# Kernel optimization log

Measured on AMD Instinct MI355X. Metric: run time of the kernel, lower is better.

The kernel has to match this reference:

```python
import jax, jax.numpy as jnp
import numpy as np

B, K, C, H, W = 16, 32, 256, 80, 80
NH, HD = 8, 32          # num_heads, head_dim (C = NH*HD)
S = 4                   # fixed roi_align sampling grid per 1x1 output bin
EPS = 1e-5


def _bn(x, g, b, m, v):
    # inference-mode BatchNorm2d, NCHW
    s = g / jnp.sqrt(v + EPS)
    return x * s[None, :, None, None] + (b - m * s)[None, :, None, None]


def _bilinear(feat, ys, xs):
    # feat [B,C,H,W]; ys,xs [B,K,S,S] -> [B,K,S,S,C], torchvision roi_align semantics
    Hh, Ww = feat.shape[2], feat.shape[3]
    valid = (ys >= -1.0) & (ys <= Hh) & (xs >= -1.0) & (xs <= Ww)
    y = jnp.clip(ys, 0.0, Hh - 1.0)
    x = jnp.clip(xs, 0.0, Ww - 1.0)
    y0 = jnp.floor(y); x0 = jnp.floor(x)
    y0i = y0.astype(jnp.int32); x0i = x0.astype(jnp.int32)
    y1i = jnp.minimum(y0i + 1, Hh - 1); x1i = jnp.minimum(x0i + 1, Ww - 1)
    ly = y - y0; lx = x - x0; hy = 1.0 - ly; hx = 1.0 - lx
    bidx = jnp.arange(feat.shape[0])[:, None, None, None]
    g = lambda yi, xi: feat[bidx, :, yi, xi]  # -> [B,K,S,S,C]
    val = ((hy * hx)[..., None] * g(y0i, x0i) + (hy * lx)[..., None] * g(y0i, x1i)
           + (ly * hx)[..., None] * g(y1i, x0i) + (ly * lx)[..., None] * g(y1i, x1i))
    return val * valid[..., None].astype(val.dtype)


def _roi_align_1x1(feat, boxes):
    # boxes [B,K,4] normalized xyxy; spatial_scale = 1.0 in the source
    Hh, Ww = feat.shape[2], feat.shape[3]
    sc = jnp.asarray([Ww - 1, Hh - 1, Ww - 1, Hh - 1], feat.dtype)
    ab = boxes * sc
    x1, y1, x2, y2 = ab[..., 0], ab[..., 1], ab[..., 2], ab[..., 3]
    rw = jnp.maximum(x2 - x1, 1.0)
    rh = jnp.maximum(y2 - y1, 1.0)
    grid = (jnp.arange(S, dtype=feat.dtype) + 0.5) / S
    ys = y1[..., None] + grid * rh[..., None]   # [B,K,S]
    xs = x1[..., None] + grid * rw[..., None]
    ys2, xs2 = jnp.broadcast_arrays(ys[..., :, None], xs[..., None, :])  # [B,K,S,S]
    vals = _bilinear(feat, ys2, xs2)            # [B,K,S,S,C]
    return vals.mean(axis=(2, 3)).reshape(feat.shape[0] * boxes.shape[1], -1)


def _gat(nodes, wq, bq, wk, bkp, wv, bv, scale, wo, bo, ln_g, ln_b):
    Bk = nodes.shape[0]
    q = (nodes @ wq.T + bq).reshape(Bk, NH, HD)
    k = (nodes @ wk.T + bkp).reshape(Bk, NH, HD)
    v = (nodes @ wv.T + bv).reshape(Bk, NH, HD)
    scores = jnp.einsum('ihd,jhd->ijh', q, k) * scale
    attn = jax.nn.softmax(scores, axis=1)       # softmax over keys j
    msg = jnp.einsum('ijh,jhd->ihd', attn, v).reshape(Bk, NH * HD)
    y = nodes + msg @ wo.T + bo
    mu = y.mean(-1, keepdims=True)
    var = ((y - mu) ** 2).mean(-1, keepdims=True)
    return (y - mu) / jnp.sqrt(var + EPS) * ln_g + ln_b


def _forward(x, boxes, conv_w, conv_b, bn1_g, bn1_b, bn1_m, bn1_v,
             wq, bq, wk, bkp, wv, bv, scale, wo, bo, ln_g, ln_b,
             rec_w, rec_b, bn2_g, bn2_b, bn2_m, bn2_v):
    feat = jax.lax.conv_general_dilated(
        x, conv_w, (1, 1), 'SAME',
        dimension_numbers=('NCHW', 'OIHW', 'NCHW')) + conv_b[None, :, None, None]
    feat = _bn(feat, bn1_g, bn1_b, bn1_m, bn1_v)
    feat = feat * jax.nn.sigmoid(feat)          # SiLU
    nodes = _roi_align_1x1(feat, boxes)         # [B*K, C]
    enh = _gat(nodes, wq, bq, wk, bkp, wv, bv, scale, wo, bo, ln_g, ln_b)
    f = enh.reshape(B, K, C)
    wts = jax.nn.softmax(f.mean(-1), axis=1)    # [B,K]
    weighted = jnp.einsum('bkc,bk->bc', f, wts)
    # out map is spatially constant -> 1x1 conv + BN collapse to per-sample affine
    y = weighted @ rec_w[:, :, 0, 0].T + rec_b
    s = bn2_g / jnp.sqrt(bn2_v + EPS)
    y = y * s + (bn2_b - bn2_m * s)
    return x + y[:, :, None, None]


def setup_inputs() -> dict:
    key = jax.random.key(0)
    ks = jax.random.split(key, 10)
    x = jax.random.normal(ks[0], (B, C, H, W), jnp.float32)
    bx = jax.random.uniform(ks[1], (B, K, 4), jnp.float32)
    bx = bx.at[:, :, 2:].add(bx[:, :, :2])      # xy2 += xy1
    boxes = jnp.clip(bx, 0.0, 1.0)
    w = lambda k, shp: jax.random.normal(k, shp, jnp.float32) * 0.02
    return {
        'x': x, 'boxes': boxes,
        'conv_w': w(ks[2], (C, C, 3, 3)), 'conv_b': jnp.zeros((C,), jnp.float32),
        'bn1_g': jnp.ones((C,), jnp.float32), 'bn1_b': jnp.zeros((C,), jnp.float32),
        'bn1_m': jnp.zeros((C,), jnp.float32), 'bn1_v': jnp.ones((C,), jnp.float32),
        'wq': w(ks[3], (C, C)), 'bq': jnp.zeros((C,), jnp.float32),
        'wk': w(ks[4], (C, C)), 'bkp': jnp.zeros((C,), jnp.float32),
        'wv': w(ks[5], (C, C)), 'bv': jnp.zeros((C,), jnp.float32),
        'scale': jnp.asarray(1.0 / np.sqrt(HD), jnp.float32),
        'wo': w(ks[6], (C, C)), 'bo': jnp.zeros((C,), jnp.float32),
        'ln_g': jnp.ones((C,), jnp.float32), 'ln_b': jnp.zeros((C,), jnp.float32),
        'rec_w': w(ks[7], (C, C, 1, 1)), 'rec_b': jnp.zeros((C,), jnp.float32),
        'bn2_g': jnp.ones((C,), jnp.float32), 'bn2_b': jnp.zeros((C,), jnp.float32),
        'bn2_m': jnp.zeros((C,), jnp.float32), 'bn2_v': jnp.ones((C,), jnp.float32),
    }


def reference(x, boxes, conv_w, conv_b, bn1_g, bn1_b, bn1_m, bn1_v,
              wq, bq, wk, bkp, wv, bv, scale, wo, bo, ln_g, ln_b,
              rec_w, rec_b, bn2_g, bn2_b, bn2_m, bn2_v):
    return _forward(x, boxes, conv_w, conv_b, bn1_g, bn1_b, bn1_m, bn1_v,
                    wq, bq, wk, bkp, wv, bv, scale, wo, bo, ln_g, ln_b,
                    rec_w, rec_b, bn2_g, bn2_b, bn2_m, bn2_v)
```

## Files before the change

### kernel.cpp

```cpp
#include <hip/hip_runtime.h>

#define EPSV 1e-5f

typedef __attribute__((ext_vector_type(8))) short short8v;
typedef __attribute__((ext_vector_type(4))) float f32x4;

static __device__ __forceinline__ unsigned short f2bf(float f) {
  unsigned int u = __float_as_uint(f);
  u += 0x7fff + ((u >> 16) & 1);
  return (unsigned short)(u >> 16);
}
static __device__ __forceinline__ float bf2f(unsigned short h) {
  return __uint_as_float(((unsigned int)h) << 16);
}

static __device__ __forceinline__ void glds16(const void* g, void* l) {
  __builtin_amdgcn_global_load_lds(
      (const __attribute__((address_space(1))) void*)g,
      (__attribute__((address_space(3))) void*)l, 16, 0, 0);
}

__global__ __launch_bounds__(256) void prep_convw_kernel(
    const float* __restrict__ cw, unsigned short* __restrict__ Wr,
    float* __restrict__ zpad)
{
  if (blockIdx.x == 0) zpad[threadIdx.x] = 0.f;
  int idx = blockIdx.x * 256 + threadIdx.x;
  if (idx >= 9 * 8 * 256 * 32) return;
  int cil = idx & 31;
  int rest = idx >> 5;
  int co = rest & 255;
  int tcc = rest >> 8;
  int cc = tcc & 7;
  int t = tcc >> 3;
  int dy = t / 3, dx = t - dy * 3;
  int ci = cc * 32 + cil;
  Wr[idx] = f2bf(cw[((co * 256 + ci) * 3 + dy) * 3 + dx]);
}

__global__ __launch_bounds__(256) void prep_transpose_kernel(
    const float* __restrict__ wq, const float* __restrict__ wk,
    const float* __restrict__ wv, const float* __restrict__ wo,
    const float* __restrict__ rec, float* __restrict__ wT)
{
  int idx = blockIdx.x * 256 + threadIdx.x;
  if (idx >= 5 * 65536) return;
  int m = idx >> 16;
  int e = idx & 65535;
  int ci = e >> 8, co = e & 255;
  const float* src = (m == 0) ? wq : (m == 1) ? wk : (m == 2) ? wv : (m == 3) ? wo : rec;
  wT[idx] = src[co * 256 + ci];
}

__global__ __launch_bounds__(256) void prep_nhwc_kernel(
    const float* __restrict__ x, unsigned short* __restrict__ xin)
{
  int blk = blockIdx.x;
  int b = blk / 80, y = blk - b * 80;
  __shared__ unsigned short t[80 * 257];
  const float* src = x + (size_t)b * 256 * 6400 + y * 80;
  for (int e = threadIdx.x; e < 256 * 20; e += 256) {
    int c = e / 20;
    int px4 = e - c * 20;
    f32x4 v = *(const f32x4*)&src[(size_t)c * 6400 + px4 * 4];
#pragma unroll
    for (int j = 0; j < 4; ++j)
      t[(px4 * 4 + j) * 257 + c] = f2bf(v[j]);
  }
  __syncthreads();
  unsigned short* dst = xin + (size_t)blk * 80 * 256;
  for (int e = threadIdx.x; e < 80 * 32; e += 256) {
    int px = e >> 5;
    int c8 = e & 31;
    short8v v;
#pragma unroll
    for (int j = 0; j < 8; ++j) v[j] = t[px * 257 + c8 * 8 + j];
    *(short8v*)&dst[px * 256 + c8 * 8] = v;
  }
}

__global__ __launch_bounds__(256, 2) void roiconv_kernel(
    const unsigned short* __restrict__ xin,
    const float* __restrict__ boxes,
    const float* __restrict__ convb,
    const float* __restrict__ bn1g, const float* __restrict__ bn1b,
    const float* __restrict__ bn1m, const float* __restrict__ bn1v,
    const unsigned short* __restrict__ Wr,
    float* __restrict__ nodes)
{
  const int bid = blockIdx.x;
  const int n = (bid & 7) * 64 + (bid >> 3);
  const int b = n >> 5;
  const int tid = threadIdx.x;
  const int w = tid >> 6, lane = tid & 63;
  const int bq = lane >> 4, r16 = lane & 15;

  __shared__ __align__(16) char lds[65792];
  float* wcoef = (float*)(lds + 65536);
  const int IN0 = 0, IN1 = 4096, W0 = 8192, W1 = 24576;

  const int px = tid >> 2;
  const float* bx = boxes + n * 4;
  float x1 = bx[0] * 79.f, y1 = bx[1] * 79.f, x2 = bx[2] * 79.f, y2 = bx[3] * 79.f;
  float rwd = fmaxf(x2 - x1, 1.f), rh = fmaxf(y2 - y1, 1.f);
  int s = px >> 2;
  int sy = s >> 2, sx = s & 3;
  float yy = y1 + (sy + 0.5f) * 0.25f * rh;
  float xx = x1 + (sx + 0.5f) * 0.25f * rwd;
  bool valid = (yy >= -1.f) && (yy <= 80.f) && (xx >= -1.f) && (xx <= 80.f);
  float yc = fminf(fmaxf(yy, 0.f), 79.f), xc = fminf(fmaxf(xx, 0.f), 79.f);
  float y0f = floorf(yc), x0f = floorf(xc);
  int y0i = (int)y0f, x0i = (int)x0f;
  int y1i = min(y0i + 1, 79), x1i = min(x0i + 1, 79);
  float ly = yc - y0f, lx = xc - x0f, hy = 1.f - ly, hx = 1.f - lx;
  int py = (px & 2) ? y1i : y0i;
  int pxx = (px & 1) ? x1i : x0i;
  if ((tid & 3) == 0)
    wcoef[px] = ((px & 2) ? ly : hy) * ((px & 1) ? lx : hx) *
                (valid ? 0.0625f : 0.f);

  const int chunk = (tid & 3) ^ ((px >> 1) & 3);
  unsigned ioff[9];
#pragma unroll
  for (int t = 0; t < 9; ++t) {
    int dy = t / 3, dx = t - dy * 3;
    int cy = py + dy - 1, cx = pxx + dx - 1;
    bool ok = ((unsigned)cy < 80u) && ((unsigned)cx < 80u);
    ioff[t] = ok ? (unsigned)((((b * 80 + cy) * 80 + cx) * 256 + chunk * 8) * 2)
                 : 52428800u;
  }
  unsigned woff[4];
#pragma unroll
  for (int i = 0; i < 4; ++i) {
    int s2 = tid + (i << 8);
    int wco = s2 >> 2;
    int wch = (s2 & 3) ^ ((wco >> 1) & 3);
    woff[i] = (unsigned)((wco * 32 + wch * 8) * 2);
  }
  const int laneoff = r16 * 64 + ((bq ^ ((r16 >> 1) & 3)) << 4);
  const char* xinb = (const char*)xin;
  const char* Wrb = (const char*)Wr;

  f32x4 acc[4][4];
#pragma unroll
  for (int i = 0; i < 4; ++i)
#pragma unroll
    for (int j = 0; j < 4; ++j)
      acc[i][j] = (f32x4){0.f, 0.f, 0.f, 0.f};

  glds16(xinb + ioff[0], lds + IN0 + ((w << 6) << 4));
#pragma unroll
  for (int i = 0; i < 4; ++i)
    glds16(Wrb + woff[i], lds + W0 + (((i << 8) + (w << 6)) << 4));
  __syncthreads();

  for (int cc = 0; cc < 8; ++cc) {
#pragma unroll
    for (int t = 0; t < 9; ++t) {
      const int step = cc * 9 + t;
      const char* inb = lds + ((step & 1) ? IN1 : IN0);
      const char* wb  = lds + ((step & 1) ? W1 : W0);
      char* innx = lds + ((step & 1) ? IN0 : IN1);
      char* wbn  = lds + ((step & 1) ? W0 : W1);
      if (step < 71) {
        const int nt = (t == 8) ? 0 : t + 1;
        const int ncc = (t == 8) ? cc + 1 : cc;
        glds16(xinb + ioff[nt] + ncc * 64, innx + ((w << 6) << 4));
        const char* wg = Wrb + ((size_t)(nt * 8 + ncc) << 14);
#pragma unroll
        for (int i = 0; i < 4; ++i)
          glds16(wg + woff[i], wbn + (((i << 8) + (w << 6)) << 4));
      }
      const char* pa = inb + laneoff;
      const char* pw = wb + w * 4096 + laneoff;
      short8v af0 = *(const short8v*)(pa);
      short8v af1 = *(const short8v*)(pa + 1024);
      short8v af2 = *(const short8v*)(pa + 2048);
      short8v af3 = *(const short8v*)(pa + 3072);
      short8v wf0 = *(const short8v*)(pw);
      short8v wf1 = *(const short8v*)(pw + 1024);
      short8v wf2 = *(const short8v*)(pw + 2048);
      short8v wf3 = *(const short8v*)(pw + 3072);
      __builtin_amdgcn_s_setprio(1);
      acc[0][0] = __builtin_amdgcn_mfma_f32_16x16x32_bf16(af0, wf0, acc[0][0], 0, 0, 0);
      acc[0][1] = __builtin_amdgcn_mfma_f32_16x16x32_bf16(af0, wf1, acc[0][1], 0, 0, 0);
      acc[0][2] = __builtin_amdgcn_mfma_f32_16x16x32_bf16(af0, wf2, acc[0][2], 0, 0, 0);
      acc[0][3] = __builtin_amdgcn_mfma_f32_16x16x32_bf16(af0, wf3, acc[0][3], 0, 0, 0);
      acc[1][0] = __builtin_amdgcn_mfma_f32_16x16x32_bf16(af1, wf0, acc[1][0], 0, 0, 0);
      acc[1][1] = __builtin_amdgcn_mfma_f32_16x16x32_bf16(af1, wf1, acc[1][1], 0, 0, 0);
      acc[1][2] = __builtin_amdgcn_mfma_f32_16x16x32_bf16(af1, wf2, acc[1][2], 0, 0, 0);
      acc[1][3] = __builtin_amdgcn_mfma_f32_16x16x32_bf16(af1, wf3, acc[1][3], 0, 0, 0);
      acc[2][0] = __builtin_amdgcn_mfma_f32_16x16x32_bf16(af2, wf0, acc[2][0], 0, 0, 0);
      acc[2][1] = __builtin_amdgcn_mfma_f32_16x16x32_bf16(af2, wf1, acc[2][1], 0, 0, 0);
      acc[2][2] = __builtin_amdgcn_mfma_f32_16x16x32_bf16(af2, wf2, acc[2][2], 0, 0, 0);
      acc[2][3] = __builtin_amdgcn_mfma_f32_16x16x32_bf16(af2, wf3, acc[2][3], 0, 0, 0);
      acc[3][0] = __builtin_amdgcn_mfma_f32_16x16x32_bf16(af3, wf0, acc[3][0], 0, 0, 0);
      acc[3][1] = __builtin_amdgcn_mfma_f32_16x16x32_bf16(af3, wf1, acc[3][1], 0, 0, 0);
      acc[3][2] = __builtin_amdgcn_mfma_f32_16x16x32_bf16(af3, wf2, acc[3][2], 0, 0, 0);
      acc[3][3] = __builtin_amdgcn_mfma_f32_16x16x32_bf16(af3, wf3, acc[3][3], 0, 0, 0);
      __builtin_amdgcn_s_setprio(0);
      __syncthreads();
    }
  }

  float* epf = (float*)lds;
#pragma unroll
  for (int cf = 0; cf < 4; ++cf) {
    int co = w * 64 + cf * 16 + r16;
    float sc = bn1g[co] / sqrtf(bn1v[co] + EPSV);
    float sh = bn1b[co] - bn1m[co] * sc;
    float cb = convb[co];
#pragma unroll
    for (int mf = 0; mf < 4; ++mf) {
#pragma unroll
      for (int rg = 0; rg < 4; ++rg) {
        int pxo = mf * 16 + bq * 4 + rg;
        float v = (acc[mf][cf][rg] + cb) * sc + sh;
        v = v / (1.f + __expf(-v));
        epf[pxo * 256 + co] = v;
      }
    }
  }
  __syncthreads();
  const int c = tid;
  float val = 0.f;
#pragma unroll
  for (int p = 0; p < 64; ++p)
    val += wcoef[p] * epf[p * 256 + c];
  nodes[n * 256 + c] = val;
}

__global__ __launch_bounds__(256) void qkv_kernel(
    const float* __restrict__ nodes, const float* __restrict__ wT,
    const float* __restrict__ bq, const float* __restrict__ bk,
    const float* __restrict__ bv,
    float* __restrict__ q, float* __restrict__ k, float* __restrict__ v)
{
  const int blk = blockIdx.x;
  const int co = threadIdx.x;
  __shared__ float nd[8][256];
  for (int i = threadIdx.x; i < 2048; i += 256)
    nd[i >> 8][i & 255] = nodes[blk * 2048 + i];
  __syncthreads();
  float aq[8] = {0,0,0,0,0,0,0,0};
  float ak[8] = {0,0,0,0,0,0,0,0};
  float av[8] = {0,0,0,0,0,0,0,0};
  const float* wqT = wT;
  const float* wkT = wT + 65536;
  const float* wvT = wT + 131072;
  for (int ci = 0; ci < 256; ++ci) {
    float wq_ = wqT[ci * 256 + co];
    float wk_ = wkT[ci * 256 + co];
    float wv_ = wvT[ci * 256 + co];
#pragma unroll
    for (int r = 0; r < 8; ++r) {
      float nv = nd[r][ci];
      aq[r] += nv * wq_;
      ak[r] += nv * wk_;
      av[r] += nv * wv_;
    }
  }
  float bq_ = bq[co], bk_ = bk[co], bv_ = bv[co];
#pragma unroll
  for (int r = 0; r < 8; ++r) {
    int n = blk * 8 + r;
    q[n * 256 + co] = aq[r] + bq_;
    k[n * 256 + co] = ak[r] + bk_;
    v[n * 256 + co] = av[r] + bv_;
  }
}

__global__ __launch_bounds__(256) void attn_kernel(
    const float* __restrict__ q, const float* __restrict__ k,
    const float* __restrict__ v, const float* __restrict__ nodes,
    const float* __restrict__ woT, const float* __restrict__ bo,
    const float* __restrict__ lng, const float* __restrict__ lnb,
    const float* __restrict__ scale_p, float* __restrict__ enh)
{
  const int i = blockIdx.x;
  const int tid = threadIdx.x;
  const float scale = scale_p[0];
  __shared__ __align__(16) float qs[256];
  __shared__ float sc[512 * 8];
  __shared__ float msgs[256];
  __shared__ float r1[4], r2[4];
  qs[tid] = q[i * 256 + tid];
  __syncthreads();
  {
    const int h = tid & 7, jl = tid >> 3;
    for (int jc = 0; jc < 16; ++jc) {
      int j = jc * 32 + jl;
      const f32x4* kr = (const f32x4*)(k + (size_t)j * 256 + h * 32);
      const f32x4* qr = (const f32x4*)(qs + h * 32);
      float s = 0.f;
#pragma unroll
      for (int d4 = 0; d4 < 8; ++d4) {
        f32x4 kv = kr[d4], qv = qr[d4];
        s += kv.x * qv.x + kv.y * qv.y + kv.z * qv.z + kv.w * qv.w;
      }
      sc[j * 8 + h] = s * scale;
    }
  }
  __syncthreads();
  const int hh = tid >> 5, l32 = tid & 31;
  float mx = -1e30f;
  for (int j = l32; j < 512; j += 32) mx = fmaxf(mx, sc[j * 8 + hh]);
#pragma unroll
  for (int o = 1; o < 32; o <<= 1) mx = fmaxf(mx, __shfl_xor(mx, o, 32));
  float sum = 0.f;
  for (int j = l32; j < 512; j += 32) {
    float e = __expf(sc[j * 8 + hh] - mx);
    sc[j * 8 + hh] = e;
    sum += e;
  }
#pragma unroll
  for (int o = 1; o < 32; o <<= 1) sum += __shfl_xor(sum, o, 32);
  float inv = 1.f / sum;
  __syncthreads();
  {
    const int d = l32;
    float m = 0.f;
    for (int j = 0; j < 512; ++j)
      m += sc[j * 8 + hh] * v[(size_t)j * 256 + hh * 32 + d];
    msgs[hh * 32 + d] = m * inv;
  }
  __syncthreads();
  const int co = tid;
  float yv = nodes[i * 256 + co] + bo[co];
  for (int ci = 0; ci < 256; ++ci)
    yv += msgs[ci] * woT[ci * 256 + co];
  float s1 = yv, s2 = yv * yv;
#pragma unroll
  for (int o = 1; o < 64; o <<= 1) { s1 += __shfl_xor(s1, o); s2 += __shfl_xor(s2, o); }
  if ((tid & 63) == 0) { r1[tid >> 6] = s1; r2[tid >> 6] = s2; }
  __syncthreads();
  float S1 = r1[0] + r1[1] + r1[2] + r1[3];
  float S2 = r2[0] + r2[1] + r2[2] + r2[3];
  float mu = S1 * (1.f / 256.f);
  float var = S2 * (1.f / 256.f) - mu * mu;
  float nrm = (yv - mu) * rsqrtf(var + EPSV);
  enh[i * 256 + co] = nrm * lng[co] + lnb[co];
}

__global__ __launch_bounds__(256) void final_kernel(
    const float* __restrict__ enh, const float* __restrict__ recT,
    const float* __restrict__ recb,
    const float* __restrict__ bn2g, const float* __restrict__ bn2b,
    const float* __restrict__ bn2m, const float* __restrict__ bn2v,
    float* __restrict__ yfin)
{
  const int b = blockIdx.x;
  const int tid = threadIdx.x;
  const int wv = tid >> 6, l = tid & 63;
  __shared__ float rm[32], wts[32], wgt[256];
  for (int kk = wv; kk < 32; kk += 4) {
    const float* er = enh + (size_t)(b * 32 + kk) * 256;
    float s = er[l] + er[l + 64] + er[l + 128] + er[l + 192];
#pragma unroll
    for (int o = 1; o < 64; o <<= 1) s += __shfl_xor(s, o);
    if (l == 0) rm[kk] = s * (1.f / 256.f);
  }
  __syncthreads();
  if (tid < 32) {
    float m = rm[tid];
    float mx = m;
#pragma unroll
    for (int o = 1; o < 32; o <<= 1) mx = fmaxf(mx, __shfl_xor(mx, o, 32));
    float e = __expf(m - mx);
    float sm = e;
#pragma unroll
    for (int o = 1; o < 32; o <<= 1) sm += __shfl_xor(sm, o, 32);
    wts[tid] = e / sm;
  }
  __syncthreads();
  float wsum = 0.f;
  for (int kk = 0; kk < 32; ++kk)
    wsum += enh[(size_t)(b * 32 + kk) * 256 + tid] * wts[kk];
  wgt[tid] = wsum;
  __syncthreads();
  const int co = tid;
  float yv = recb[co];
  for (int ci = 0; ci < 256; ++ci)
    yv += wgt[ci] * recT[ci * 256 + co];
  float s = bn2g[co] / sqrtf(bn2v[co] + EPSV);
  yfin[b * 256 + co] = yv * s + (bn2b[co] - bn2m[co] * s);
}

__global__ __launch_bounds__(256) void add_kernel(
    const float* __restrict__ x, const float* __restrict__ yfin,
    float* __restrict__ out)
{
  const int bc = blockIdx.x;
  const float a = yfin[bc];
  const f32x4* xp = (const f32x4*)(x + (size_t)bc * 6400);
  f32x4* op = (f32x4*)(out + (size_t)bc * 6400);
  for (int i = threadIdx.x; i < 1600; i += 256) {
    f32x4 v = xp[i];
    v.x += a; v.y += a; v.z += a; v.w += a;
    op[i] = v;
  }
}

extern "C" void kernel_launch(void* const* d_in, const int* in_sizes, int n_in,
                              void* d_out, int out_size, void* d_ws, size_t ws_size,
                              hipStream_t stream)
{
  const float* x      = (const float*)d_in[0];
  const float* boxes  = (const float*)d_in[1];
  const float* conv_w = (const float*)d_in[2];
  const float* conv_b = (const float*)d_in[3];
  const float* bn1g   = (const float*)d_in[4];
  const float* bn1b   = (const float*)d_in[5];
  const float* bn1m   = (const float*)d_in[6];
  const float* bn1v   = (const float*)d_in[7];
  const float* wq     = (const float*)d_in[8];
  const float* bq     = (const float*)d_in[9];
  const float* wk     = (const float*)d_in[10];
  const float* bkp    = (const float*)d_in[11];
  const float* wv     = (const float*)d_in[12];
  const float* bv     = (const float*)d_in[13];
  const float* scale  = (const float*)d_in[14];
  const float* wo     = (const float*)d_in[15];
  const float* bo     = (const float*)d_in[16];
  const float* lng    = (const float*)d_in[17];
  const float* lnb    = (const float*)d_in[18];
  const float* rec_w  = (const float*)d_in[19];
  const float* rec_b  = (const float*)d_in[20];
  const float* bn2g   = (const float*)d_in[21];
  const float* bn2b   = (const float*)d_in[22];
  const float* bn2m   = (const float*)d_in[23];
  const float* bn2v   = (const float*)d_in[24];
  float* out = (float*)d_out;

  char* ws = (char*)d_ws;
  unsigned short* Wr   = (unsigned short*)(ws);
  float* wT    = (float*)(ws + 53608448);
  float* nodes = (float*)(ws + 54919168);
  float* qb    = nodes + 131072;
  float* kb    = qb + 131072;
  float* vb    = kb + 131072;
  float* enh   = vb + 131072;
  float* yfin  = enh + 131072;

  unsigned short* xin = (unsigned short*)d_out;
  float* zpad = (float*)((char*)d_out + 52428800);

  hipLaunchKernelGGL(prep_convw_kernel, dim3(2304), dim3(256), 0, stream,
                     conv_w, Wr, zpad);
  hipLaunchKernelGGL(prep_transpose_kernel, dim3(1280), dim3(256), 0, stream,
                     wq, wk, wv, wo, rec_w, wT);
  hipLaunchKernelGGL(prep_nhwc_kernel, dim3(1280), dim3(256), 0, stream, x, xin);
  hipLaunchKernelGGL(roiconv_kernel, dim3(512), dim3(256), 0, stream,
                     xin, boxes, conv_b, bn1g, bn1b, bn1m, bn1v, Wr, nodes);
  hipLaunchKernelGGL(qkv_kernel, dim3(64), dim3(256), 0, stream,
                     nodes, wT, bq, bkp, bv, qb, kb, vb);
  hipLaunchKernelGGL(attn_kernel, dim3(512), dim3(256), 0, stream,
                     qb, kb, vb, nodes, wT + 3 * 65536, bo, lng, lnb, scale, enh);
  hipLaunchKernelGGL(final_kernel, dim3(16), dim3(256), 0, stream,
                     enh, wT + 4 * 65536, rec_b, bn2g, bn2b, bn2m, bn2v, yfin);
  hipLaunchKernelGGL(add_kernel, dim3(4096), dim3(256), 0, stream, x, yfin, out);
}
```

Before: 208.0 us.

## Fuse prep kernels, shrink roiconv LDS, split attention into per-head and out-proj kernels

Merges the three preprocessing kernels into one launch that dispatches on block index. The roiconv epilogue buffer is stored as bf16 with a padded stride, which cuts shared memory so three blocks can fit per CU. The per-query attention kernel is replaced by a per-head kernel that stages K/V for 16 queries in swizzled LDS. A separate kernel then handles the output projection and LayerNorm over 8 rows per block. The trade-offs are an extra launch, a msgs buffer round trip through memory, and bf16 rounding of the softmax probabilities and epilogue activations.

```diff
diff --git a/kernel.cpp b/kernel.cpp
--- a/kernel.cpp
+++ b/kernel.cpp
@@ -20,66 +20,61 @@
       (__attribute__((address_space(3))) void*)l, 16, 0, 0);
 }
 
-__global__ __launch_bounds__(256) void prep_convw_kernel(
+__global__ __launch_bounds__(256) void prep_fused_kernel(
+    const float* __restrict__ x, unsigned short* __restrict__ xin,
     const float* __restrict__ cw, unsigned short* __restrict__ Wr,
-    float* __restrict__ zpad)
-{
-  if (blockIdx.x == 0) zpad[threadIdx.x] = 0.f;
-  int idx = blockIdx.x * 256 + threadIdx.x;
-  if (idx >= 9 * 8 * 256 * 32) return;
-  int cil = idx & 31;
-  int rest = idx >> 5;
-  int co = rest & 255;
-  int tcc = rest >> 8;
-  int cc = tcc & 7;
-  int t = tcc >> 3;
-  int dy = t / 3, dx = t - dy * 3;
-  int ci = cc * 32 + cil;
-  Wr[idx] = f2bf(cw[((co * 256 + ci) * 3 + dy) * 3 + dx]);
-}
-
-__global__ __launch_bounds__(256) void prep_transpose_kernel(
+    float* __restrict__ zpad,
     const float* __restrict__ wq, const float* __restrict__ wk,
     const float* __restrict__ wv, const float* __restrict__ wo,
     const float* __restrict__ rec, float* __restrict__ wT)
 {
-  int idx = blockIdx.x * 256 + threadIdx.x;
-  if (idx >= 5 * 65536) return;
-  int m = idx >> 16;
-  int e = idx & 65535;
-  int ci = e >> 8, co = e & 255;
-  const float* src = (m == 0) ? wq : (m == 1) ? wk : (m == 2) ? wv : (m == 3) ? wo : rec;
-  wT[idx] = src[co * 256 + ci];
-}
-
-__global__ __launch_bounds__(256) void prep_nhwc_kernel(
-    const float* __restrict__ x, unsigned short* __restrict__ xin)
-{
-  int blk = blockIdx.x;
-  int b = blk / 80, y = blk - b * 80;
   __shared__ unsigned short t[80 * 257];
-  const float* src = x + (size_t)b * 256 * 6400 + y * 80;
-  for (int e = threadIdx.x; e < 256 * 20; e += 256) {
-    int c = e / 20;
-    int px4 = e - c * 20;
-    f32x4 v = *(const f32x4*)&src[(size_t)c * 6400 + px4 * 4];
-#pragma unroll
-    for (int j = 0; j < 4; ++j)
-      t[(px4 * 4 + j) * 257 + c] = f2bf(v[j]);
-  }
-  __syncthreads();
-  unsigned short* dst = xin + (size_t)blk * 80 * 256;
-  for (int e = threadIdx.x; e < 80 * 32; e += 256) {
-    int px = e >> 5;
-    int c8 = e & 31;
-    short8v v;
-#pragma unroll
-    for (int j = 0; j < 8; ++j) v[j] = t[px * 257 + c8 * 8 + j];
-    *(short8v*)&dst[px * 256 + c8 * 8] = v;
-  }
-}
-
-__global__ __launch_bounds__(256, 2) void roiconv_kernel(
+  const int bid = blockIdx.x;
+  if (bid < 1280) {
+    int b = bid / 80, y = bid - b * 80;
+    const float* src = x + (size_t)b * 256 * 6400 + y * 80;
+    for (int e = threadIdx.x; e < 256 * 20; e += 256) {
+      int c = e / 20;
+      int px4 = e - c * 20;
+      f32x4 v = *(const f32x4*)&src[(size_t)c * 6400 + px4 * 4];
+#pragma unroll
+      for (int j = 0; j < 4; ++j)
+        t[(px4 * 4 + j) * 257 + c] = f2bf(v[j]);
+    }
+    __syncthreads();
+    unsigned short* dst = xin + (size_t)bid * 80 * 256;
+    for (int e = threadIdx.x; e < 80 * 32; e += 256) {
+      int px = e >> 5;
+      int c8 = e & 31;
+      short8v v;
+#pragma unroll
+      for (int j = 0; j < 8; ++j) v[j] = t[px * 257 + c8 * 8 + j];
+      *(short8v*)&dst[px * 256 + c8 * 8] = v;
+    }
+  } else if (bid < 3584) {
+    if (bid == 1280) zpad[threadIdx.x] = 0.f;
+    int idx = (bid - 1280) * 256 + threadIdx.x;
+    int cil = idx & 31;
+    int rest = idx >> 5;
+    int co = rest & 255;
+    int tcc = rest >> 8;
+    int cc = tcc & 7;
+    int tt = tcc >> 3;
+    int dy = tt / 3, dx = tt - dy * 3;
+    int ci = cc * 32 + cil;
+    Wr[idx] = f2bf(cw[((co * 256 + ci) * 3 + dy) * 3 + dx]);
+  } else {
+    int idx = (bid - 3584) * 256 + threadIdx.x;
+    int m = idx >> 16;
+    int e = idx & 65535;
+    int ci = e >> 8, co = e & 255;
+    const float* src = (m == 0) ? wq : (m == 1) ? wk : (m == 2) ? wv
+                     : (m == 3) ? wo : rec;
+    wT[idx] = src[co * 256 + ci];
+  }
+}
+
+__global__ __launch_bounds__(256, 3) void roiconv_kernel(
     const unsigned short* __restrict__ xin,
     const float* __restrict__ boxes,
     const float* __restrict__ convb,
@@ -95,8 +90,8 @@
   const int w = tid >> 6, lane = tid & 63;
   const int bq = lane >> 4, r16 = lane & 15;
 
-  __shared__ __align__(16) char lds[65792];
-  float* wcoef = (float*)(lds + 65536);
+  __shared__ __align__(16) char lds[41216];
+  float* wcoef = (float*)(lds + 40960);
   const int IN0 = 0, IN1 = 4096, W0 = 8192, W1 = 24576;
 
   const int px = tid >> 2;
@@ -203,7 +198,7 @@
     }
   }
 
-  float* epf = (float*)lds;
+  unsigned short* ep = (unsigned short*)lds;
 #pragma unroll
   for (int cf = 0; cf < 4; ++cf) {
     int co = w * 64 + cf * 16 + r16;
@@ -217,7 +212,7 @@
         int pxo = mf * 16 + bq * 4 + rg;
         float v = (acc[mf][cf][rg] + cb) * sc + sh;
         v = v / (1.f + __expf(-v));
-        epf[pxo * 256 + co] = v;
+        ep[pxo * 264 + co] = f2bf(v);
       }
     }
   }
@@ -226,7 +221,7 @@
   float val = 0.f;
 #pragma unroll
   for (int p = 0; p < 64; ++p)
-    val += wcoef[p] * epf[p * 256 + c];
+    val += wcoef[p] * bf2f(ep[p * 264 + c]);
   nodes[n * 256 + c] = val;
 }
 
@@ -270,76 +265,128 @@
   }
 }
 
-__global__ __launch_bounds__(256) void attn_kernel(
+__global__ __launch_bounds__(256) void attn_mh_kernel(
     const float* __restrict__ q, const float* __restrict__ k,
-    const float* __restrict__ v, const float* __restrict__ nodes,
+    const float* __restrict__ v, const float* __restrict__ scale_p,
+    float* __restrict__ msgs)
+{
+  const int bid = blockIdx.x;
+  const int h = bid & 7, qc = bid >> 3;
+  const int q0 = qc * 16;
+  const int tid = threadIdx.x;
+  __shared__ __align__(16) float Kh[512 * 32];
+  __shared__ __align__(16) float Vh[512 * 32];
+  __shared__ unsigned short pb[16 * 512];
+
+  for (int idx = tid; idx < 4096; idx += 256) {
+    int j = idx >> 3, part = idx & 7;
+    int chs = part ^ (j & 7);
+    *(f32x4*)&Kh[j * 32 + chs * 4] =
+        *(const f32x4*)&k[(size_t)j * 256 + h * 32 + part * 4];
+    *(f32x4*)&Vh[j * 32 + chs * 4] =
+        *(const f32x4*)&v[(size_t)j * 256 + h * 32 + part * 4];
+  }
+  const int qi = tid >> 4, l = tid & 15;
+  f32x4 qr[8];
+#pragma unroll
+  for (int p = 0; p < 8; ++p)
+    qr[p] = *(const f32x4*)&q[(size_t)(q0 + qi) * 256 + h * 32 + p * 4];
+  const float scale = scale_p[0];
+  __syncthreads();
+
+  float pj[32];
+  float mx = -1e30f;
+#pragma unroll
+  for (int jj = 0; jj < 32; ++jj) {
+    int j = jj * 16 + l;
+    const float* kr = &Kh[j * 32];
+    int sw = j & 7;
+    float s = 0.f;
+#pragma unroll
+    for (int p = 0; p < 8; ++p) {
+      f32x4 kv = *(const f32x4*)&kr[(p ^ sw) * 4];
+      s += kv.x * qr[p].x + kv.y * qr[p].y + kv.z * qr[p].z + kv.w * qr[p].w;
+    }
+    s *= scale;
+    pj[jj] = s;
+    mx = fmaxf(mx, s);
+  }
+#pragma unroll
+  for (int o = 1; o < 16; o <<= 1) mx = fmaxf(mx, __shfl_xor(mx, o, 16));
+  float sum = 0.f;
+#pragma unroll
+  for (int jj = 0; jj < 32; ++jj) {
+    float e = __expf(pj[jj] - mx);
+    pj[jj] = e;
+    sum += e;
+  }
+#pragma unroll
+  for (int o = 1; o < 16; o <<= 1) sum += __shfl_xor(sum, o, 16);
+  float inv = 1.f / sum;
+#pragma unroll
+  for (int jj = 0; jj < 32; ++jj)
+    pb[qi * 512 + jj * 16 + l] = f2bf(pj[jj] * inv);
+  __syncthreads();
+
+  float m0 = 0.f, m1 = 0.f;
+  const unsigned short* pq = &pb[qi * 512];
+  for (int j = 0; j < 512; ++j) {
+    float p = bf2f(pq[j]);
+    int chs = (l >> 1) ^ (j & 7);
+    const float* vr = &Vh[j * 32 + chs * 4 + ((2 * l) & 3)];
+    m0 += p * vr[0];
+    m1 += p * vr[1];
+  }
+  float* mo = &msgs[(size_t)(q0 + qi) * 256 + h * 32 + 2 * l];
+  mo[0] = m0;
+  mo[1] = m1;
+}
+
+__global__ __launch_bounds__(256) void outln_kernel(
+    const float* __restrict__ msgs, const float* __restrict__ nodes,
     const float* __restrict__ woT, const float* __restrict__ bo,
     const float* __restrict__ lng, const float* __restrict__ lnb,
-    const float* __restrict__ scale_p, float* __restrict__ enh)
-{
-  const int i = blockIdx.x;
-  const int tid = threadIdx.x;
-  const float scale = scale_p[0];
-  __shared__ __align__(16) float qs[256];
-  __shared__ float sc[512 * 8];
-  __shared__ float msgs[256];
-  __shared__ float r1[4], r2[4];
-  qs[tid] = q[i * 256 + tid];
-  __syncthreads();
-  {
-    const int h = tid & 7, jl = tid >> 3;
-    for (int jc = 0; jc < 16; ++jc) {
-      int j = jc * 32 + jl;
-      const f32x4* kr = (const f32x4*)(k + (size_t)j * 256 + h * 32);
-      const f32x4* qr = (const f32x4*)(qs + h * 32);
-      float s = 0.f;
-#pragma unroll
-      for (int d4 = 0; d4 < 8; ++d4) {
-        f32x4 kv = kr[d4], qv = qr[d4];
-        s += kv.x * qv.x + kv.y * qv.y + kv.z * qv.z + kv.w * qv.w;
-      }
-      sc[j * 8 + h] = s * scale;
-    }
-  }
-  __syncthreads();
-  const int hh = tid >> 5, l32 = tid & 31;
-  float mx = -1e30f;
-  for (int j = l32; j < 512; j += 32) mx = fmaxf(mx, sc[j * 8 + hh]);
-#pragma unroll
-  for (int o = 1; o < 32; o <<= 1) mx = fmaxf(mx, __shfl_xor(mx, o, 32));
-  float sum = 0.f;
-  for (int j = l32; j < 512; j += 32) {
-    float e = __expf(sc[j * 8 + hh] - mx);
-    sc[j * 8 + hh] = e;
-    sum += e;
-  }
-#pragma unroll
-  for (int o = 1; o < 32; o <<= 1) sum += __shfl_xor(sum, o, 32);
-  float inv = 1.f / sum;
-  __syncthreads();
-  {
-    const int d = l32;
-    float m = 0.f;
-    for (int j = 0; j < 512; ++j)
-      m += sc[j * 8 + hh] * v[(size_t)j * 256 + hh * 32 + d];
-    msgs[hh * 32 + d] = m * inv;
-  }
-  __syncthreads();
-  const int co = tid;
-  float yv = nodes[i * 256 + co] + bo[co];
-  for (int ci = 0; ci < 256; ++ci)
-    yv += msgs[ci] * woT[ci * 256 + co];
-  float s1 = yv, s2 = yv * yv;
-#pragma unroll
-  for (int o = 1; o < 64; o <<= 1) { s1 += __shfl_xor(s1, o); s2 += __shfl_xor(s2, o); }
-  if ((tid & 63) == 0) { r1[tid >> 6] = s1; r2[tid >> 6] = s2; }
-  __syncthreads();
-  float S1 = r1[0] + r1[1] + r1[2] + r1[3];
-  float S2 = r2[0] + r2[1] + r2[2] + r2[3];
-  float mu = S1 * (1.f / 256.f);
-  float var = S2 * (1.f / 256.f) - mu * mu;
-  float nrm = (yv - mu) * rsqrtf(var + EPSV);
-  enh[i * 256 + co] = nrm * lng[co] + lnb[co];
+    float* __restrict__ enh)
+{
+  const int blk = blockIdx.x;
+  const int co = threadIdx.x;
+  __shared__ float ms[8][256];
+  __shared__ float red1[8][4], red2[8][4];
+  for (int i = co; i < 2048; i += 256)
+    ms[i >> 8][i & 255] = msgs[blk * 2048 + i];
+  __syncthreads();
+  float yv[8];
+  float bo_ = bo[co];
+#pragma unroll
+  for (int r = 0; r < 8; ++r)
+    yv[r] = nodes[(size_t)(blk * 8 + r) * 256 + co] + bo_;
+  for (int ci = 0; ci < 256; ++ci) {
+    float w = woT[ci * 256 + co];
+#pragma unroll
+    for (int r = 0; r < 8; ++r) yv[r] += ms[r][ci] * w;
+  }
+  const int wv = co >> 6, lane = co & 63;
+#pragma unroll
+  for (int r = 0; r < 8; ++r) {
+    float s1 = yv[r], s2 = yv[r] * yv[r];
+#pragma unroll
+    for (int o = 1; o < 64; o <<= 1) {
+      s1 += __shfl_xor(s1, o);
+      s2 += __shfl_xor(s2, o);
+    }
+    if (lane == 0) { red1[r][wv] = s1; red2[r][wv] = s2; }
+  }
+  __syncthreads();
+  float lg = lng[co], lb = lnb[co];
+#pragma unroll
+  for (int r = 0; r < 8; ++r) {
+    float S1 = red1[r][0] + red1[r][1] + red1[r][2] + red1[r][3];
+    float S2 = red2[r][0] + red2[r][1] + red2[r][2] + red2[r][3];
+    float mu = S1 * (1.f / 256.f);
+    float var = S2 * (1.f / 256.f) - mu * mu;
+    enh[(size_t)(blk * 8 + r) * 256 + co] =
+        (yv[r] - mu) * rsqrtf(var + EPSV) * lg + lb;
+  }
 }
 
 __global__ __launch_bounds__(256) void final_kernel(
@@ -433,7 +480,7 @@
   float* out = (float*)d_out;
 
   char* ws = (char*)d_ws;
-  unsigned short* Wr   = (unsigned short*)(ws);
+  unsigned short* Wr = (unsigned short*)(ws);
   float* wT    = (float*)(ws + 53608448);
   float* nodes = (float*)(ws + 54919168);
   float* qb    = nodes + 131072;
@@ -441,21 +488,21 @@
   float* vb    = kb + 131072;
   float* enh   = vb + 131072;
   float* yfin  = enh + 131072;
+  float* msgs  = yfin + 4096;
 
   unsigned short* xin = (unsigned short*)d_out;
   float* zpad = (float*)((char*)d_out + 52428800);
 
-  hipLaunchKernelGGL(prep_convw_kernel, dim3(2304), dim3(256), 0, stream,
-                     conv_w, Wr, zpad);
-  hipLaunchKernelGGL(prep_transpose_kernel, dim3(1280), dim3(256), 0, stream,
-                     wq, wk, wv, wo, rec_w, wT);
-  hipLaunchKernelGGL(prep_nhwc_kernel, dim3(1280), dim3(256), 0, stream, x, xin);
+  hipLaunchKernelGGL(prep_fused_kernel, dim3(4864), dim3(256), 0, stream,
+                     x, xin, conv_w, Wr, zpad, wq, wk, wv, wo, rec_w, wT);
   hipLaunchKernelGGL(roiconv_kernel, dim3(512), dim3(256), 0, stream,
                      xin, boxes, conv_b, bn1g, bn1b, bn1m, bn1v, Wr, nodes);
   hipLaunchKernelGGL(qkv_kernel, dim3(64), dim3(256), 0, stream,
                      nodes, wT, bq, bkp, bv, qb, kb, vb);
-  hipLaunchKernelGGL(attn_kernel, dim3(512), dim3(256), 0, stream,
-                     qb, kb, vb, nodes, wT + 3 * 65536, bo, lng, lnb, scale, enh);
+  hipLaunchKernelGGL(attn_mh_kernel, dim3(256), dim3(256), 0, stream,
+                     qb, kb, vb, scale, msgs);
+  hipLaunchKernelGGL(outln_kernel, dim3(64), dim3(256), 0, stream,
+                     msgs, nodes, wT + 3 * 65536, bo, lng, lnb, enh);
   hipLaunchKernelGGL(final_kernel, dim3(16), dim3(256), 0, stream,
                      enh, wT + 4 * 65536, rec_b, bn2g, bn2b, bn2m, bn2v, yfin);
   hipLaunchKernelGGL(add_kernel, dim3(4096), dim3(256), 0, stream, x, yfin, out);
```

Result: faster. 190.1 us (-8.6%).
